# Performance work log

Hardware: AMD Instinct MI355X
Metric: run time of the kernel (lower is better)

The kernel has to match this reference:

```python
import jax, jax.numpy as jnp
import numpy as np

B, S, D_IN, D_OUT, R = 8, 2048, 2048, 2048, 16

def setup_inputs() -> dict:
    key = jax.random.key(0)
    k = jax.random.split(key, 5)
    scale_w = 1.0 / np.sqrt(D_IN)
    return {
        "x": jax.random.normal(k[0], (B, S, D_IN), dtype=jnp.float32),
        "A_params": jax.random.normal(k[1], (B, D_OUT, R), dtype=jnp.float32) * 0.02,
        "B_params": jax.random.normal(k[2], (B, R, D_IN), dtype=jnp.float32) * 0.02,
        "W": jax.random.normal(k[3], (D_OUT, D_IN), dtype=jnp.float32) * scale_w,
        "b": jax.random.normal(k[4], (D_OUT,), dtype=jnp.float32) * scale_w,
    }

def reference(x, A_params, B_params, W, b):
    # base: x @ W^T + b  -> [B, S, out]
    base_out = jnp.einsum("bsi,oi->bso", x, W) + b
    # intermediate = x @ B^T -> [B, S, r]
    intermediate = jnp.einsum("bsi,bri->bsr", x, B_params)
    # adaptation = intermediate @ A^T -> [B, S, out]
    adaptation = jnp.einsum("bsr,bor->bso", intermediate, A_params)
    return base_out + adaptation
```

## Files before the change

kernel.cpp:

```cpp
#include <hip/hip_runtime.h>
#include <cstdint>
#include <cstddef>

typedef __attribute__((ext_vector_type(4))) float  floatx4;
typedef __attribute__((ext_vector_type(8))) __bf16 bf16x8;
typedef __attribute__((ext_vector_type(8))) unsigned short u16x8;

#define M_TOT 16384
#define N_TOT 2048
#define K_TOT 2048
#define NBATCH 8
#define RLORA 16
#define NT 32

__device__ __forceinline__ unsigned short f32_to_bf16(float f) {
  unsigned u = __float_as_uint(f);
  u += 0x7fffu + ((u >> 16) & 1u);
  return (unsigned short)(u >> 16);
}

#define GLOAD_LDS16(gp, lp)                                                        \
  __builtin_amdgcn_global_load_lds((__attribute__((address_space(1))) void*)(void*)(gp), \
                                   (__attribute__((address_space(3))) void*)(void*)(lp), \
                                   16, 0, 0)

template<int V> struct IC { static constexpr int value = V; };

__global__ void k_convert(const float* __restrict__ in, unsigned short* __restrict__ out, int n8) {
  int i = blockIdx.x * blockDim.x + threadIdx.x;
  if (i >= n8) return;
  const float4* p = (const float4*)in + (size_t)i * 2;
  float4 v0 = p[0], v1 = p[1];
  u16x8 o;
  o[0] = f32_to_bf16(v0.x); o[1] = f32_to_bf16(v0.y);
  o[2] = f32_to_bf16(v0.z); o[3] = f32_to_bf16(v0.w);
  o[4] = f32_to_bf16(v1.x); o[5] = f32_to_bf16(v1.y);
  o[6] = f32_to_bf16(v1.z); o[7] = f32_to_bf16(v1.w);
  *(u16x8*)(out + (size_t)i * 8) = o;
}

__global__ void k_convert_a(const float* __restrict__ A, unsigned short* __restrict__ abf) {
  int row = blockIdx.x * blockDim.x + threadIdx.x;
  if (row >= NBATCH * N_TOT) return;
  const float4* p = (const float4*)(A + (size_t)row * RLORA);
  float4 v0 = p[0], v1 = p[1], v2 = p[2], v3 = p[3];
  u16x8 lo, hi2, z = {0,0,0,0,0,0,0,0};
  lo[0] = f32_to_bf16(v0.x); lo[1] = f32_to_bf16(v0.y);
  lo[2] = f32_to_bf16(v0.z); lo[3] = f32_to_bf16(v0.w);
  lo[4] = f32_to_bf16(v1.x); lo[5] = f32_to_bf16(v1.y);
  lo[6] = f32_to_bf16(v1.z); lo[7] = f32_to_bf16(v1.w);
  hi2[0] = f32_to_bf16(v2.x); hi2[1] = f32_to_bf16(v2.y);
  hi2[2] = f32_to_bf16(v2.z); hi2[3] = f32_to_bf16(v2.w);
  hi2[4] = f32_to_bf16(v3.x); hi2[5] = f32_to_bf16(v3.y);
  hi2[6] = f32_to_bf16(v3.z); hi2[7] = f32_to_bf16(v3.w);
  u16x8* dst = (u16x8*)(abf + (size_t)row * 32);
  dst[0] = lo; dst[1] = hi2; dst[2] = z; dst[3] = z;
}

__global__ __launch_bounds__(256) void k_inter(const unsigned short* __restrict__ xbf,
                                               const unsigned short* __restrict__ bpbf,
                                               unsigned short* __restrict__ interbf) {
  const int tid  = threadIdx.x;
  const int lane = tid & 63;
  const int wv   = tid >> 6;
  const int l15  = lane & 15;
  const int hi   = lane >> 4;
  const int m0   = blockIdx.x * 64;
  const int bb   = m0 >> 11;

  floatx4 zero = {0.f, 0.f, 0.f, 0.f};
  floatx4 acc[4] = {zero, zero, zero, zero};

  const unsigned short* bpb = bpbf + (size_t)bb * (RLORA * K_TOT);
  const int kb0 = wv * 512;
  for (int kb = kb0; kb < kb0 + 512; kb += 32) {
    bf16x8 bfr = *(const bf16x8*)(bpb + (size_t)l15 * K_TOT + kb + hi * 8);
    #pragma unroll
    for (int mi = 0; mi < 4; ++mi) {
      bf16x8 afr = *(const bf16x8*)(xbf + (size_t)(m0 + mi * 16 + l15) * K_TOT + kb + hi * 8);
      acc[mi] = __builtin_amdgcn_mfma_f32_16x16x32_bf16(afr, bfr, acc[mi], 0, 0, 0);
    }
  }

  __shared__ floatx4 red[4][4][64];
  #pragma unroll
  for (int mi = 0; mi < 4; ++mi) red[wv][mi][lane] = acc[mi];
  __syncthreads();
  if (wv == 0) {
    #pragma unroll
    for (int mi = 0; mi < 4; ++mi) {
      floatx4 s = red[0][mi][lane] + red[1][mi][lane] + red[2][mi][lane] + red[3][mi][lane];
      #pragma unroll
      for (int j = 0; j < 4; ++j) {
        int m = m0 + mi * 16 + hi * 4 + j;
        interbf[(size_t)m * 32 + l15] = f32_to_bf16(s[j]);
        interbf[(size_t)m * 32 + 16 + l15] = 0;
      }
    }
  }
}

#define STAGE_A(bufi, h, tt) do {                                                      \
  GLOAD_LDS16(Ag + (h)*262144 + (tt)*64 + gOff0, AsB + ((bufi)*2+(h))*16384 + ldsB0);  \
  GLOAD_LDS16(Ag + (h)*262144 + (tt)*64 + gOff1, AsB + ((bufi)*2+(h))*16384 + ldsB1);  \
} while(0)
#define STAGE_B(bufi, h, tt) do {                                                      \
  GLOAD_LDS16(Bg + (h)*262144 + (tt)*64 + gOff0, BsB + ((bufi)*2+(h))*16384 + ldsB0);  \
  GLOAD_LDS16(Bg + (h)*262144 + (tt)*64 + gOff1, BsB + ((bufi)*2+(h))*16384 + ldsB1);  \
} while(0)
#define RDA_(B2, qm, mi, ks) (*(const bf16x8*)(AsB + (B2)*32768 + aBase + (qm)*8192 + (mi)*2048 + koff[ks]))
#define RDB_(B2, ni, ks)     (*(const bf16x8*)(BsB + (B2)*32768 + bBase + (ni)*2048 + koff[ks]))
#define BAR() __builtin_amdgcn_s_barrier()
#define MFMA16(MB, NB, AF, BF) do {                                                        \
  _Pragma("unroll")                                                                        \
  for (int mi = 0; mi < 4; ++mi) {                                                         \
    _Pragma("unroll")                                                                      \
    for (int j = 0; j < 2; ++j) {                                                          \
      acc[(MB)+mi][(NB)+j] = __builtin_amdgcn_mfma_f32_16x16x32_bf16(AF[mi][0], BF[j][0], acc[(MB)+mi][(NB)+j], 0, 0, 0); \
      acc[(MB)+mi][(NB)+j] = __builtin_amdgcn_mfma_f32_16x16x32_bf16(AF[mi][1], BF[j][1], acc[(MB)+mi][(NB)+j], 0, 0, 0); \
    }                                                                                      \
  }                                                                                        \
} while(0)

__global__ __launch_bounds__(512, 2) void k_gemm(const unsigned short* __restrict__ xbf,
                                                 const unsigned short* __restrict__ wbf,
                                                 const unsigned short* __restrict__ interbf,
                                                 const unsigned short* __restrict__ abf,
                                                 const float* __restrict__ bias,
                                                 float* __restrict__ out) {
  __shared__ unsigned short As[2][2][8192];
  __shared__ unsigned short Bs[2][2][8192];
  const int tid  = threadIdx.x;
  const int lane = tid & 63;
  const int wid  = tid >> 6;
  const int wm   = wid >> 2;
  const int wn   = wid & 3;
  const int l15  = lane & 15;
  const int hi   = lane >> 4;
  const int swz  = l15 & 7;

  int bid  = blockIdx.x;
  int swzb = ((bid & 7) << 6) | (bid >> 3);
  const int mt = swzb >> 3;
  const int nt = swzb & 7;
  const int mrow0 = mt << 8;
  const int ncol0 = nt << 8;
  const int bb = mrow0 >> 11;

  const int m0 = mrow0 + wm * 128;
  const int n0 = ncol0 + wn * 64;

  const unsigned short* Ag = xbf + (size_t)mrow0 * K_TOT;
  const unsigned short* Bg = wbf + (size_t)ncol0 * K_TOT;
  char* AsB = (char*)As;
  char* BsB = (char*)Bs;

  const int r0    = tid >> 3;
  const int k80   = (tid & 7) ^ (r0 & 7);
  const int gOff0 = r0 * K_TOT + k80 * 8;
  const int gOff1 = gOff0 + 64 * K_TOT;
  const int ldsB0 = wid * 1024;
  const int ldsB1 = 8192 + wid * 1024;

  const int aBase = wm * 16384 + l15 * 128;
  const int bBase = wn * 8192  + l15 * 128;
  int koff[2];
  koff[0] = ((0 * 4 + hi) ^ swz) * 16;
  koff[1] = ((1 * 4 + hi) ^ swz) * 16;

  floatx4 acc[8][4];
  bf16x8 afA[4][2], afB[4][2], bfP[2][2], bfQ[2][2];

  {
    bf16x8 la[8], lb[4];
    #pragma unroll
    for (int mi = 0; mi < 8; ++mi)
      la[mi] = *(const bf16x8*)(interbf + (size_t)(m0 + mi * 16 + l15) * 32 + hi * 8);
    #pragma unroll
    for (int ni = 0; ni < 4; ++ni)
      lb[ni] = *(const bf16x8*)(abf + ((size_t)bb * N_TOT + n0 + ni * 16 + l15) * 32 + hi * 8);

    STAGE_B(0, 0, 0); STAGE_B(0, 1, 0); STAGE_A(0, 0, 0); STAGE_A(0, 1, 0);
    STAGE_B(1, 0, 1); STAGE_B(1, 1, 1); STAGE_A(1, 0, 1);

    floatx4 z = {0.f, 0.f, 0.f, 0.f};
    #pragma unroll
    for (int mi = 0; mi < 8; ++mi)
      #pragma unroll
      for (int ni = 0; ni < 4; ++ni)
        acc[mi][ni] = __builtin_amdgcn_mfma_f32_16x16x32_bf16(la[mi], lb[ni], z, 0, 0, 0);
  }
  asm volatile("s_waitcnt vmcnt(6)" ::: "memory");
  BAR();
  #pragma unroll
  for (int mi = 0; mi < 4; ++mi) { afA[mi][0] = RDA_(0, 0, mi, 0); afA[mi][1] = RDA_(0, 0, mi, 1); }
  #pragma unroll
  for (int j = 0; j < 2; ++j)    { bfP[j][0]  = RDB_(0, j, 0);     bfP[j][1]  = RDB_(0, j, 1); }

  auto tile_step = [&](int t, auto bufc, auto s1c, auto s2c, auto vmc, auto lastc,
                       auto& bfF, auto& bfS) {
    constexpr int BUF  = decltype(bufc)::value;
    constexpr int S1   = decltype(s1c)::value;
    constexpr int S2   = decltype(s2c)::value;
    constexpr int VM   = decltype(vmc)::value;
    constexpr int LAST = decltype(lastc)::value;

    #pragma unroll
    for (int j = 0; j < 2; ++j) { bfS[j][0] = RDB_(BUF, 2 + j, 0); bfS[j][1] = RDB_(BUF, 2 + j, 1); }
    if constexpr (S1) STAGE_A(BUF ^ 1, 1, t + 1);
    BAR();
    asm volatile("s_waitcnt lgkmcnt(4)" ::: "memory");
    __builtin_amdgcn_s_setprio(1);
    MFMA16(0, 0, afA, bfF);
    __builtin_amdgcn_s_setprio(0);
    BAR();

    #pragma unroll
    for (int mi = 0; mi < 4; ++mi) { afB[mi][0] = RDA_(BUF, 1, mi, 0); afB[mi][1] = RDA_(BUF, 1, mi, 1); }
    BAR();
    asm volatile("s_waitcnt lgkmcnt(8)" ::: "memory");
    __builtin_amdgcn_s_setprio(1);
    MFMA16(0, 2, afA, bfS);
    __builtin_amdgcn_s_setprio(0);
    BAR();

    if constexpr (S2) { STAGE_B(BUF, 0, t + 2); STAGE_B(BUF, 1, t + 2); }
    BAR();
    asm volatile("s_waitcnt lgkmcnt(0)" ::: "memory");
    __builtin_amdgcn_s_setprio(1);
    MFMA16(4, 2, afB, bfS);
    __builtin_amdgcn_s_setprio(0);
    if constexpr (VM == 4)      asm volatile("s_waitcnt vmcnt(4)" ::: "memory");
    else if constexpr (VM == 0) asm volatile("s_waitcnt vmcnt(0)" ::: "memory");
    BAR();

    if constexpr (!LAST) {
      #pragma unroll
      for (int mi = 0; mi < 4; ++mi) { afA[mi][0] = RDA_(BUF ^ 1, 0, mi, 0); afA[mi][1] = RDA_(BUF ^ 1, 0, mi, 1); }
      #pragma unroll
      for (int j = 0; j < 2; ++j)    { bfS[j][0] = RDB_(BUF ^ 1, j, 0);      bfS[j][1] = RDB_(BUF ^ 1, j, 1); }
    }
    if constexpr (S2) STAGE_A(BUF, 0, t + 2);
    BAR();
    __builtin_amdgcn_s_setprio(1);
    MFMA16(4, 0, afB, bfF);
    __builtin_amdgcn_s_setprio(0);
    BAR();
  };

  for (int t = 0; t < NT - 2; t += 2) {
    tile_step(t,     IC<0>{}, IC<1>{}, IC<1>{}, IC<4>{}, IC<0>{}, bfP, bfQ);
    tile_step(t + 1, IC<1>{}, IC<1>{}, IC<1>{}, IC<4>{}, IC<0>{}, bfQ, bfP);
  }
  tile_step(NT - 2, IC<0>{}, IC<1>{}, IC<0>{}, IC<0>{},  IC<0>{}, bfP, bfQ);
  tile_step(NT - 1, IC<1>{}, IC<0>{}, IC<0>{}, IC<-1>{}, IC<1>{}, bfQ, bfP);

  #pragma unroll
  for (int ni = 0; ni < 4; ++ni) {
    int col = n0 + ni * 16 + l15;
    float bv = bias[col];
    #pragma unroll
    for (int mi = 0; mi < 8; ++mi) {
      int r = m0 + mi * 16 + hi * 4;
      #pragma unroll
      for (int j = 0; j < 4; ++j)
        out[(size_t)(r + j) * N_TOT + col] = acc[mi][ni][j] + bv;
    }
  }
}

extern "C" void kernel_launch(void* const* d_in, const int* in_sizes, int n_in,
                              void* d_out, int out_size, void* d_ws, size_t ws_size,
                              hipStream_t stream) {
  const float* x    = (const float*)d_in[0];
  const float* Ap   = (const float*)d_in[1];
  const float* Bp   = (const float*)d_in[2];
  const float* W    = (const float*)d_in[3];
  const float* bias = (const float*)d_in[4];
  float* out = (float*)d_out;

  char* ws = (char*)d_ws;
  unsigned short* xbf     = (unsigned short*)(ws);
  unsigned short* wbf     = (unsigned short*)(ws + 67108864);
  unsigned short* abf     = (unsigned short*)(ws + 67108864 + 8388608);
  unsigned short* bpbf    = (unsigned short*)(ws + 67108864 + 8388608 + 1048576);
  unsigned short* interbf = (unsigned short*)(ws + 67108864 + 8388608 + 1048576 + 524288);

  k_convert<<<dim3(16384), dim3(256), 0, stream>>>(x,  xbf,  4194304);
  k_convert<<<dim3(2048),  dim3(256), 0, stream>>>(W,  wbf,   524288);
  k_convert<<<dim3(128),   dim3(256), 0, stream>>>(Bp, bpbf,   32768);
  k_convert_a<<<dim3(64),  dim3(256), 0, stream>>>(Ap, abf);

  k_inter<<<dim3(256), dim3(256), 0, stream>>>(xbf, bpbf, interbf);

  k_gemm<<<dim3(512), dim3(512), 0, stream>>>(xbf, wbf, interbf, abf, bias, out);
}
```

Before: 198.8 us.

## Merge small conversion kernels and restructure GEMM main loop into four A sub-tile phases

Folds the three small fp32-to-bf16 conversions (W, B, A) into one launch and makes the x conversion do eight elements per thread, cutting launch count and tail effects. The GEMM inner loop is rewritten: each wave loads all four B fragments once per k-tile and walks A in four 32-row quarters, issuing next-tile A and B staging between phases. This changes the LDS B layout indexing and the prefetch schedule, and uses lgkmcnt(0) waits before every MFMA phase, which may expose more LDS latency in exchange for fewer live fragment registers.

```diff
diff --git a/kernel.cpp b/kernel.cpp
--- a/kernel.cpp
+++ b/kernel.cpp
@@ -19,6 +19,15 @@
   return (unsigned short)(u >> 16);
 }
 
+__device__ __forceinline__ u16x8 cvt8(const float4& a, const float4& b) {
+  u16x8 o;
+  o[0] = f32_to_bf16(a.x); o[1] = f32_to_bf16(a.y);
+  o[2] = f32_to_bf16(a.z); o[3] = f32_to_bf16(a.w);
+  o[4] = f32_to_bf16(b.x); o[5] = f32_to_bf16(b.y);
+  o[6] = f32_to_bf16(b.z); o[7] = f32_to_bf16(b.w);
+  return o;
+}
+
 #define GLOAD_LDS16(gp, lp)                                                        \
   __builtin_amdgcn_global_load_lds((__attribute__((address_space(1))) void*)(void*)(gp), \
                                    (__attribute__((address_space(3))) void*)(void*)(lp), \
@@ -26,35 +35,36 @@
 
 template<int V> struct IC { static constexpr int value = V; };
 
-__global__ void k_convert(const float* __restrict__ in, unsigned short* __restrict__ out, int n8) {
-  int i = blockIdx.x * blockDim.x + threadIdx.x;
-  if (i >= n8) return;
-  const float4* p = (const float4*)in + (size_t)i * 2;
-  float4 v0 = p[0], v1 = p[1];
-  u16x8 o;
-  o[0] = f32_to_bf16(v0.x); o[1] = f32_to_bf16(v0.y);
-  o[2] = f32_to_bf16(v0.z); o[3] = f32_to_bf16(v0.w);
-  o[4] = f32_to_bf16(v1.x); o[5] = f32_to_bf16(v1.y);
-  o[6] = f32_to_bf16(v1.z); o[7] = f32_to_bf16(v1.w);
-  *(u16x8*)(out + (size_t)i * 8) = o;
-}
-
-__global__ void k_convert_a(const float* __restrict__ A, unsigned short* __restrict__ abf) {
-  int row = blockIdx.x * blockDim.x + threadIdx.x;
-  if (row >= NBATCH * N_TOT) return;
-  const float4* p = (const float4*)(A + (size_t)row * RLORA);
-  float4 v0 = p[0], v1 = p[1], v2 = p[2], v3 = p[3];
-  u16x8 lo, hi2, z = {0,0,0,0,0,0,0,0};
-  lo[0] = f32_to_bf16(v0.x); lo[1] = f32_to_bf16(v0.y);
-  lo[2] = f32_to_bf16(v0.z); lo[3] = f32_to_bf16(v0.w);
-  lo[4] = f32_to_bf16(v1.x); lo[5] = f32_to_bf16(v1.y);
-  lo[6] = f32_to_bf16(v1.z); lo[7] = f32_to_bf16(v1.w);
-  hi2[0] = f32_to_bf16(v2.x); hi2[1] = f32_to_bf16(v2.y);
-  hi2[2] = f32_to_bf16(v2.z); hi2[3] = f32_to_bf16(v2.w);
-  hi2[4] = f32_to_bf16(v3.x); hi2[5] = f32_to_bf16(v3.y);
-  hi2[6] = f32_to_bf16(v3.z); hi2[7] = f32_to_bf16(v3.w);
-  u16x8* dst = (u16x8*)(abf + (size_t)row * 32);
-  dst[0] = lo; dst[1] = hi2; dst[2] = z; dst[3] = z;
+__global__ void k_convert_x(const float* __restrict__ in, unsigned short* __restrict__ out) {
+  int i0 = blockIdx.x * blockDim.x + threadIdx.x;
+  #pragma unroll
+  for (int it = 0; it < 8; ++it) {
+    size_t i = (size_t)i0 + (size_t)it * 524288;
+    const float4* p = (const float4*)in + i * 2;
+    *(u16x8*)(out + i * 8) = cvt8(p[0], p[1]);
+  }
+}
+
+__global__ void k_convert_small(const float* __restrict__ W, const float* __restrict__ Bp,
+                                const float* __restrict__ Ap,
+                                unsigned short* __restrict__ wbf, unsigned short* __restrict__ bpbf,
+                                unsigned short* __restrict__ abf) {
+  int b = blockIdx.x;
+  if (b < 2048) {
+    int i = b * 256 + threadIdx.x;
+    const float4* p = (const float4*)W + (size_t)i * 2;
+    *(u16x8*)(wbf + (size_t)i * 8) = cvt8(p[0], p[1]);
+  } else if (b < 2176) {
+    int i = (b - 2048) * 256 + threadIdx.x;
+    const float4* p = (const float4*)Bp + (size_t)i * 2;
+    *(u16x8*)(bpbf + (size_t)i * 8) = cvt8(p[0], p[1]);
+  } else {
+    int row = (b - 2176) * 256 + threadIdx.x;
+    const float4* p = (const float4*)(Ap + (size_t)row * RLORA);
+    u16x8 lo = cvt8(p[0], p[1]), hi2 = cvt8(p[2], p[3]), z = {0,0,0,0,0,0,0,0};
+    u16x8* dst = (u16x8*)(abf + (size_t)row * 32);
+    dst[0] = lo; dst[1] = hi2; dst[2] = z; dst[3] = z;
+  }
 }
 
 __global__ __launch_bounds__(256) void k_inter(const unsigned short* __restrict__ xbf,
@@ -108,19 +118,9 @@
   GLOAD_LDS16(Bg + (h)*262144 + (tt)*64 + gOff0, BsB + ((bufi)*2+(h))*16384 + ldsB0);  \
   GLOAD_LDS16(Bg + (h)*262144 + (tt)*64 + gOff1, BsB + ((bufi)*2+(h))*16384 + ldsB1);  \
 } while(0)
-#define RDA_(B2, qm, mi, ks) (*(const bf16x8*)(AsB + (B2)*32768 + aBase + (qm)*8192 + (mi)*2048 + koff[ks]))
-#define RDB_(B2, ni, ks)     (*(const bf16x8*)(BsB + (B2)*32768 + bBase + (ni)*2048 + koff[ks]))
+#define RDA_(B2, q, mi, ks) (*(const bf16x8*)(AsB + (B2)*32768 + aBase + (q)*4096 + (mi)*2048 + koff[ks]))
+#define RDB_(B2, ni, ks)    (*(const bf16x8*)(BsB + (B2)*32768 + bBase + (ni)*2048 + koff[ks]))
 #define BAR() __builtin_amdgcn_s_barrier()
-#define MFMA16(MB, NB, AF, BF) do {                                                        \
-  _Pragma("unroll")                                                                        \
-  for (int mi = 0; mi < 4; ++mi) {                                                         \
-    _Pragma("unroll")                                                                      \
-    for (int j = 0; j < 2; ++j) {                                                          \
-      acc[(MB)+mi][(NB)+j] = __builtin_amdgcn_mfma_f32_16x16x32_bf16(AF[mi][0], BF[j][0], acc[(MB)+mi][(NB)+j], 0, 0, 0); \
-      acc[(MB)+mi][(NB)+j] = __builtin_amdgcn_mfma_f32_16x16x32_bf16(AF[mi][1], BF[j][1], acc[(MB)+mi][(NB)+j], 0, 0, 0); \
-    }                                                                                      \
-  }                                                                                        \
-} while(0)
 
 __global__ __launch_bounds__(512, 2) void k_gemm(const unsigned short* __restrict__ xbf,
                                                  const unsigned short* __restrict__ wbf,
@@ -163,13 +163,14 @@
   const int ldsB1 = 8192 + wid * 1024;
 
   const int aBase = wm * 16384 + l15 * 128;
-  const int bBase = wn * 8192  + l15 * 128;
+  const int bBase = (wn >> 1) * 16384 + (wn & 1) * 8192 + l15 * 128;
   int koff[2];
   koff[0] = ((0 * 4 + hi) ^ swz) * 16;
   koff[1] = ((1 * 4 + hi) ^ swz) * 16;
 
   floatx4 acc[8][4];
-  bf16x8 afA[4][2], afB[4][2], bfP[2][2], bfQ[2][2];
+  bf16x8 bfr[4][2];
+  bf16x8 af[2][2];
 
   {
     bf16x8 la[8], lb[4];
@@ -180,8 +181,8 @@
     for (int ni = 0; ni < 4; ++ni)
       lb[ni] = *(const bf16x8*)(abf + ((size_t)bb * N_TOT + n0 + ni * 16 + l15) * 32 + hi * 8);
 
-    STAGE_B(0, 0, 0); STAGE_B(0, 1, 0); STAGE_A(0, 0, 0); STAGE_A(0, 1, 0);
-    STAGE_B(1, 0, 1); STAGE_B(1, 1, 1); STAGE_A(1, 0, 1);
+    STAGE_A(0, 0, 0); STAGE_A(0, 1, 0); STAGE_B(0, 0, 0); STAGE_B(0, 1, 0);
+    STAGE_B(1, 0, 1); STAGE_B(1, 1, 1);
 
     floatx4 z = {0.f, 0.f, 0.f, 0.f};
     #pragma unroll
@@ -190,70 +191,90 @@
       for (int ni = 0; ni < 4; ++ni)
         acc[mi][ni] = __builtin_amdgcn_mfma_f32_16x16x32_bf16(la[mi], lb[ni], z, 0, 0, 0);
   }
-  asm volatile("s_waitcnt vmcnt(6)" ::: "memory");
+  asm volatile("s_waitcnt vmcnt(4)" ::: "memory");
   BAR();
-  #pragma unroll
-  for (int mi = 0; mi < 4; ++mi) { afA[mi][0] = RDA_(0, 0, mi, 0); afA[mi][1] = RDA_(0, 0, mi, 1); }
-  #pragma unroll
-  for (int j = 0; j < 2; ++j)    { bfP[j][0]  = RDB_(0, j, 0);     bfP[j][1]  = RDB_(0, j, 1); }
-
-  auto tile_step = [&](int t, auto bufc, auto s1c, auto s2c, auto vmc, auto lastc,
-                       auto& bfF, auto& bfS) {
-    constexpr int BUF  = decltype(bufc)::value;
-    constexpr int S1   = decltype(s1c)::value;
-    constexpr int S2   = decltype(s2c)::value;
-    constexpr int VM   = decltype(vmc)::value;
-    constexpr int LAST = decltype(lastc)::value;
-
-    #pragma unroll
-    for (int j = 0; j < 2; ++j) { bfS[j][0] = RDB_(BUF, 2 + j, 0); bfS[j][1] = RDB_(BUF, 2 + j, 1); }
-    if constexpr (S1) STAGE_A(BUF ^ 1, 1, t + 1);
-    BAR();
-    asm volatile("s_waitcnt lgkmcnt(4)" ::: "memory");
-    __builtin_amdgcn_s_setprio(1);
-    MFMA16(0, 0, afA, bfF);
-    __builtin_amdgcn_s_setprio(0);
-    BAR();
-
-    #pragma unroll
-    for (int mi = 0; mi < 4; ++mi) { afB[mi][0] = RDA_(BUF, 1, mi, 0); afB[mi][1] = RDA_(BUF, 1, mi, 1); }
-    BAR();
-    asm volatile("s_waitcnt lgkmcnt(8)" ::: "memory");
-    __builtin_amdgcn_s_setprio(1);
-    MFMA16(0, 2, afA, bfS);
-    __builtin_amdgcn_s_setprio(0);
-    BAR();
-
-    if constexpr (S2) { STAGE_B(BUF, 0, t + 2); STAGE_B(BUF, 1, t + 2); }
+
+  auto tile_step = [&](int t, auto bufc, auto sac, auto sbc, auto vmc) {
+    constexpr int BUF = decltype(bufc)::value;
+    constexpr int SA  = decltype(sac)::value;
+    constexpr int SB  = decltype(sbc)::value;
+    constexpr int VM  = decltype(vmc)::value;
+
+    #pragma unroll
+    for (int ni = 0; ni < 4; ++ni) { bfr[ni][0] = RDB_(BUF, ni, 0); bfr[ni][1] = RDB_(BUF, ni, 1); }
+    #pragma unroll
+    for (int mi = 0; mi < 2; ++mi) { af[mi][0] = RDA_(BUF, 0, mi, 0); af[mi][1] = RDA_(BUF, 0, mi, 1); }
+    if constexpr (SA) STAGE_A(BUF ^ 1, 0, t + 1);
     BAR();
     asm volatile("s_waitcnt lgkmcnt(0)" ::: "memory");
     __builtin_amdgcn_s_setprio(1);
-    MFMA16(4, 2, afB, bfS);
+    #pragma unroll
+    for (int mi = 0; mi < 2; ++mi)
+      #pragma unroll
+      for (int ni = 0; ni < 4; ++ni) {
+        acc[mi][ni] = __builtin_amdgcn_mfma_f32_16x16x32_bf16(af[mi][0], bfr[ni][0], acc[mi][ni], 0, 0, 0);
+        acc[mi][ni] = __builtin_amdgcn_mfma_f32_16x16x32_bf16(af[mi][1], bfr[ni][1], acc[mi][ni], 0, 0, 0);
+      }
+    __builtin_amdgcn_s_setprio(0);
+    BAR();
+
+    #pragma unroll
+    for (int mi = 0; mi < 2; ++mi) { af[mi][0] = RDA_(BUF, 1, mi, 0); af[mi][1] = RDA_(BUF, 1, mi, 1); }
+    if constexpr (SA) STAGE_A(BUF ^ 1, 1, t + 1);
+    BAR();
+    asm volatile("s_waitcnt lgkmcnt(0)" ::: "memory");
+    __builtin_amdgcn_s_setprio(1);
+    #pragma unroll
+    for (int mi = 0; mi < 2; ++mi)
+      #pragma unroll
+      for (int ni = 0; ni < 4; ++ni) {
+        acc[2+mi][ni] = __builtin_amdgcn_mfma_f32_16x16x32_bf16(af[mi][0], bfr[ni][0], acc[2+mi][ni], 0, 0, 0);
+        acc[2+mi][ni] = __builtin_amdgcn_mfma_f32_16x16x32_bf16(af[mi][1], bfr[ni][1], acc[2+mi][ni], 0, 0, 0);
+      }
+    __builtin_amdgcn_s_setprio(0);
+    BAR();
+
+    #pragma unroll
+    for (int mi = 0; mi < 2; ++mi) { af[mi][0] = RDA_(BUF, 2, mi, 0); af[mi][1] = RDA_(BUF, 2, mi, 1); }
+    if constexpr (SB) STAGE_B(BUF, 0, t + 2);
+    BAR();
+    asm volatile("s_waitcnt lgkmcnt(0)" ::: "memory");
+    __builtin_amdgcn_s_setprio(1);
+    #pragma unroll
+    for (int mi = 0; mi < 2; ++mi)
+      #pragma unroll
+      for (int ni = 0; ni < 4; ++ni) {
+        acc[4+mi][ni] = __builtin_amdgcn_mfma_f32_16x16x32_bf16(af[mi][0], bfr[ni][0], acc[4+mi][ni], 0, 0, 0);
+        acc[4+mi][ni] = __builtin_amdgcn_mfma_f32_16x16x32_bf16(af[mi][1], bfr[ni][1], acc[4+mi][ni], 0, 0, 0);
+      }
+    __builtin_amdgcn_s_setprio(0);
+    BAR();
+
+    #pragma unroll
+    for (int mi = 0; mi < 2; ++mi) { af[mi][0] = RDA_(BUF, 3, mi, 0); af[mi][1] = RDA_(BUF, 3, mi, 1); }
+    if constexpr (SB) STAGE_B(BUF, 1, t + 2);
+    BAR();
+    asm volatile("s_waitcnt lgkmcnt(0)" ::: "memory");
+    __builtin_amdgcn_s_setprio(1);
+    #pragma unroll
+    for (int mi = 0; mi < 2; ++mi)
+      #pragma unroll
+      for (int ni = 0; ni < 4; ++ni) {
+        acc[6+mi][ni] = __builtin_amdgcn_mfma_f32_16x16x32_bf16(af[mi][0], bfr[ni][0], acc[6+mi][ni], 0, 0, 0);
+        acc[6+mi][ni] = __builtin_amdgcn_mfma_f32_16x16x32_bf16(af[mi][1], bfr[ni][1], acc[6+mi][ni], 0, 0, 0);
+      }
     __builtin_amdgcn_s_setprio(0);
     if constexpr (VM == 4)      asm volatile("s_waitcnt vmcnt(4)" ::: "memory");
     else if constexpr (VM == 0) asm volatile("s_waitcnt vmcnt(0)" ::: "memory");
     BAR();
-
-    if constexpr (!LAST) {
-      #pragma unroll
-      for (int mi = 0; mi < 4; ++mi) { afA[mi][0] = RDA_(BUF ^ 1, 0, mi, 0); afA[mi][1] = RDA_(BUF ^ 1, 0, mi, 1); }
-      #pragma unroll
-      for (int j = 0; j < 2; ++j)    { bfS[j][0] = RDB_(BUF ^ 1, j, 0);      bfS[j][1] = RDB_(BUF ^ 1, j, 1); }
-    }
-    if constexpr (S2) STAGE_A(BUF, 0, t + 2);
-    BAR();
-    __builtin_amdgcn_s_setprio(1);
-    MFMA16(4, 0, afB, bfF);
-    __builtin_amdgcn_s_setprio(0);
-    BAR();
   };
 
   for (int t = 0; t < NT - 2; t += 2) {
-    tile_step(t,     IC<0>{}, IC<1>{}, IC<1>{}, IC<4>{}, IC<0>{}, bfP, bfQ);
-    tile_step(t + 1, IC<1>{}, IC<1>{}, IC<1>{}, IC<4>{}, IC<0>{}, bfQ, bfP);
-  }
-  tile_step(NT - 2, IC<0>{}, IC<1>{}, IC<0>{}, IC<0>{},  IC<0>{}, bfP, bfQ);
-  tile_step(NT - 1, IC<1>{}, IC<0>{}, IC<0>{}, IC<-1>{}, IC<1>{}, bfQ, bfP);
+    tile_step(t,     IC<0>{}, IC<1>{}, IC<1>{}, IC<4>{});
+    tile_step(t + 1, IC<1>{}, IC<1>{}, IC<1>{}, IC<4>{});
+  }
+  tile_step(NT - 2, IC<0>{}, IC<1>{}, IC<0>{}, IC<0>{});
+  tile_step(NT - 1, IC<1>{}, IC<0>{}, IC<0>{}, IC<-1>{});
 
   #pragma unroll
   for (int ni = 0; ni < 4; ++ni) {
@@ -286,12 +307,8 @@
   unsigned short* bpbf    = (unsigned short*)(ws + 67108864 + 8388608 + 1048576);
   unsigned short* interbf = (unsigned short*)(ws + 67108864 + 8388608 + 1048576 + 524288);
 
-  k_convert<<<dim3(16384), dim3(256), 0, stream>>>(x,  xbf,  4194304);
-  k_convert<<<dim3(2048),  dim3(256), 0, stream>>>(W,  wbf,   524288);
-  k_convert<<<dim3(128),   dim3(256), 0, stream>>>(Bp, bpbf,   32768);
-  k_convert_a<<<dim3(64),  dim3(256), 0, stream>>>(Ap, abf);
-
+  k_convert_small<<<dim3(2240), dim3(256), 0, stream>>>(W, Bp, Ap, wbf, bpbf, abf);
+  k_convert_x<<<dim3(2048), dim3(256), 0, stream>>>(x, xbf);
   k_inter<<<dim3(256), dim3(256), 0, stream>>>(xbf, bpbf, interbf);
-
   k_gemm<<<dim3(512), dim3(512), 0, stream>>>(xbf, wbf, interbf, abf, bias, out);
 }
```

After: 197.6 us. Within noise of the previous version (-0.6%).
